# Kernel optimization log

Measured on AMD Instinct MI355X. Metric: run time of the kernel, lower is better.

## Reference

```python
import jax, jax.numpy as jnp
import numpy as np

D = 256   # vec_dim
H = 8     # head_num
P = 1024  # patch_num
N = 8     # batch


def setup_inputs() -> dict:
    key = jax.random.key(0)
    ks = jax.random.split(key, 11)
    s = 0.05
    return {
        "inputs": jax.random.normal(ks[0], (N, D, P), dtype=jnp.float32),
        "pos_mat": jax.random.normal(ks[1], (1, H, P, P), dtype=jnp.float32),
        "Wk": jax.random.normal(ks[2], (H * D, D), dtype=jnp.float32) * s,
        "bk": jax.random.normal(ks[3], (H * D,), dtype=jnp.float32) * s,
        "Wq": jax.random.normal(ks[4], (H * D, D), dtype=jnp.float32) * s,
        "bq": jax.random.normal(ks[5], (H * D,), dtype=jnp.float32) * s,
        "Wv": jax.random.normal(ks[6], (H * D, D), dtype=jnp.float32) * s,
        "bv": jax.random.normal(ks[7], (H * D,), dtype=jnp.float32) * s,
        "Wo": jax.random.normal(ks[8], (D, H * D), dtype=jnp.float32) * s,
        "bo": jax.random.normal(ks[9], (D,), dtype=jnp.float32) * s,
    }


def reference(inputs, pos_mat, Wk, bk, Wq, bq, Wv, bv, Wo, bo):
    n, d, p = inputs.shape  # [N, D, P]
    h = Wk.shape[0] // d
    # 1x1 Conv1d == per-position GEMM: [H*D,D] x [N,D,P] -> [N,H*D,P] -> [N,H,D,P]
    k = (jnp.einsum('od,ndp->nop', Wk, inputs) + bk[:, None]).reshape(n, h, d, p)
    q = (jnp.einsum('od,ndp->nop', Wq, inputs) + bq[:, None]).reshape(n, h, d, p)
    v = (jnp.einsum('od,ndp->nop', Wv, inputs) + bv[:, None]).reshape(n, h, d, p)
    # attn[n,h,kpos,qpos] = K^T Q / sqrt(D), shape [N,H,P,P]
    attn = jnp.einsum('nhdk,nhdq->nhkq', k, q) / jnp.sqrt(jnp.asarray(d, inputs.dtype))
    attn = attn + pos_mat
    # NOTE: original uses Softmax(dim=2), i.e. over the KEY axis, not the last dim
    w = jax.nn.softmax(attn, axis=2)
    out = jnp.einsum('nhdk,nhkq->nhdq', v, w).reshape(n, h * d, p)
    return jnp.einsum('oi,nip->nop', Wo, out) + bo[:, None]
```

## Files before the change

kernel.cpp:

```cpp
#include <hip/hip_runtime.h>

typedef __bf16 bf16;
typedef __attribute__((ext_vector_type(8))) __bf16 bf16x8;
typedef __attribute__((ext_vector_type(4))) __bf16 bf16x4;
typedef __attribute__((ext_vector_type(2))) __bf16 bf16x2;
typedef __attribute__((ext_vector_type(4))) float f32x4;

#define MFMA16(a, b, c) __builtin_amdgcn_mfma_f32_16x16x32_bf16(a, b, c, 0, 0, 0)

__device__ __forceinline__ void gload_lds16(const void* g, void* l) {
  __builtin_amdgcn_global_load_lds(
      (const __attribute__((address_space(1))) void*)g,
      (__attribute__((address_space(3))) void*)l, 16, 0, 0);
}

constexpr int NH = 8, DD = 256, PP = 1024;

constexpr size_t WB_YT  = 33554432;
constexpr size_t WB_XB  = 67108864;
constexpr size_t WB_XBT = 71303168;
constexpr size_t WB_MB  = 75497472;
constexpr size_t WB_UB  = 76546048;
constexpr size_t WB_U   = 77594624;
constexpr size_t WB_BPP = 77602816;

constexpr int FL_PT0  = 0;
constexpr int FL_XT0  = 16384;
constexpr int FL_LRED = 0;
constexpr int FL_SZ   = 81920;

#define EXP_SHIFT 4.0f

__global__ __launch_bounds__(256, 1) void msa_mu(
    const float* __restrict__ Wk, const float* __restrict__ Wq,
    const float* __restrict__ Wo, const float* __restrict__ Wv,
    const float* __restrict__ bq, const float* __restrict__ bv,
    bf16* __restrict__ Mb, bf16* __restrict__ Ub,
    float* __restrict__ u, float* __restrict__ bpp) {
  __shared__ float lds[64 * 65];
  __shared__ float svec[64];
  const int t = threadIdx.x;
  const int i0 = (blockIdx.x >> 2) * 64;
  const int jq = blockIdx.x & 3;
  const int h = blockIdx.y;
  const int mode = blockIdx.z;
  const int j0 = (t & 31) * 2 + jq * 64;
  const int i8 = t >> 5;
  float acc0[8], acc1[8];
#pragma unroll
  for (int r = 0; r < 8; ++r) { acc0[r] = 0.f; acc1[r] = 0.f; }
  float accS = 0.f;
  const float* __restrict__ W2 = (mode == 0) ? Wq : Wv;
  const float* __restrict__ vec = (mode == 0) ? bq : bv;
  for (int dhc = 0; dhc < 256; dhc += 64) {
    __syncthreads();
    if (mode == 0) {
#pragma unroll
      for (int s = 0; s < 16; ++s) {
        int f = t + s * 256;
        int dh = f >> 6, ii = f & 63;
        lds[dh * 65 + ii] = Wk[(h * 256 + dhc + dh) * 256 + i0 + ii];
      }
    } else {
#pragma unroll
      for (int s = 0; s < 16; ++s) {
        int f = t + s * 256;
        int oo = f >> 6, dh = f & 63;
        lds[dh * 65 + oo] = Wo[(i0 + oo) * 2048 + h * 256 + dhc + dh];
      }
    }
    if (jq == 0 && t < 64) svec[t] = vec[h * 256 + dhc + t];
    __syncthreads();
#pragma unroll 8
    for (int dl = 0; dl < 64; ++dl) {
      float2 wv2 = *reinterpret_cast<const float2*>(&W2[(h * 256 + dhc + dl) * 256 + j0]);
#pragma unroll
      for (int r = 0; r < 8; ++r) {
        float x = lds[dl * 65 + i8 * 8 + r];
        acc0[r] = fmaf(x, wv2.x, acc0[r]);
        acc1[r] = fmaf(x, wv2.y, acc1[r]);
      }
    }
    if (jq == 0 && t < 64) {
      float a = 0.f;
#pragma unroll 8
      for (int dh = 0; dh < 64; ++dh) a = fmaf(lds[dh * 65 + t], svec[dh], a);
      accS += a;
    }
  }
  if (mode == 0) {
#pragma unroll
    for (int r = 0; r < 8; ++r) {
      int i = i0 + i8 * 8 + r;
      bf16x2 v = { (__bf16)(acc0[r] * 0.0625f), (__bf16)(acc1[r] * 0.0625f) };
      *reinterpret_cast<bf16x2*>(&Mb[h * 65536 + i * 256 + j0]) = v;
    }
    if (jq == 0 && t < 64) u[h * 256 + i0 + t] = accS * 0.0625f;
  } else {
#pragma unroll
    for (int r = 0; r < 8; ++r) {
      int o = i0 + i8 * 8 + r;
      bf16x2 v = { (__bf16)acc0[r], (__bf16)acc1[r] };
      *reinterpret_cast<bf16x2*>(&Ub[o * 2048 + h * 256 + j0]) = v;
    }
    if (jq == 0 && t < 64) bpp[h * 256 + i0 + t] = accS;
  }
}

__global__ __launch_bounds__(256, 4) void msa_cvtX(
    const float* __restrict__ X, bf16* __restrict__ Xb, bf16* __restrict__ XbT) {
  __shared__ __bf16 tl[64 * 68];
  const int t = threadIdx.x;
  const int p0 = blockIdx.x * 64, d0 = blockIdx.y * 64, n = blockIdx.z;
  const float* __restrict__ Xn = X + (size_t)n * DD * PP;
#pragma unroll
  for (int rr = 0; rr < 4; ++rr) {
    int r = (t >> 4) + rr * 16, c = (t & 15) * 4;
    float4 v = *reinterpret_cast<const float4*>(Xn + (size_t)(d0 + r) * PP + p0 + c);
    bf16x4 pk = { (__bf16)v.x, (__bf16)v.y, (__bf16)v.z, (__bf16)v.w };
    *reinterpret_cast<bf16x4*>(Xb + (size_t)n * DD * PP + (size_t)(d0 + r) * PP + p0 + c) = pk;
    *reinterpret_cast<bf16x4*>(&tl[r * 68 + c]) = pk;
  }
  __syncthreads();
#pragma unroll
  for (int rr = 0; rr < 4; ++rr) {
    int pr = (t >> 4) + rr * 16, dc = (t & 15) * 4;
    bf16x4 pk = { tl[(dc + 0) * 68 + pr], tl[(dc + 1) * 68 + pr],
                  tl[(dc + 2) * 68 + pr], tl[(dc + 3) * 68 + pr] };
    *reinterpret_cast<bf16x4*>(XbT + (size_t)n * PP * DD + (size_t)(p0 + pr) * DD + d0 + dc) = pk;
  }
}

__global__ __launch_bounds__(256, 2) void msa_flash(
    const bf16* __restrict__ XbT, const bf16* __restrict__ Xb,
    const bf16* __restrict__ Mb, const float* __restrict__ u,
    const float* __restrict__ pos, bf16* __restrict__ Yt) {
  extern __shared__ char smc[];
  const int t = threadIdx.x;
  const int lane = t & 63, w = t >> 6;
  const int g = lane >> 4, ln = lane & 15;
  const int kw = w >> 1, qw = w & 1;
  const int qt = blockIdx.x, h = blockIdx.y, n = blockIdx.z;
  const int qg0 = qt * 64, nh = n * 8 + h;
  const bf16* __restrict__ XbTn = XbT + (size_t)n * (PP * DD);
  const bf16* __restrict__ Xbn  = Xb + (size_t)n * (DD * PP);
  const bf16* __restrict__ Mh   = Mb + (size_t)h * (DD * DD);
  const float* __restrict__ posh = pos + (size_t)h * (PP * PP);
  float* lredp = (float*)(smc + FL_LRED);

  const int grl = lane >> 5;
  const int gcb = lane & 31;

  {
    bf16x8 ta[4][8];
#pragma unroll
    for (int mq = 0; mq < 4; ++mq)
#pragma unroll
      for (int s = 0; s < 8; ++s)
        ta[mq][s] = *reinterpret_cast<const bf16x8*>(
            XbTn + (size_t)(qg0 + mq * 16 + ln) * DD + s * 32 + g * 8);
#pragma unroll
    for (int ni = 0; ni < 4; ++ni) {
      const int i_ = w * 64 + ni * 16 + ln;
      bf16x8 tb8[8];
#pragma unroll
      for (int s = 0; s < 8; ++s)
        tb8[s] = *reinterpret_cast<const bf16x8*>(Mh + (size_t)i_ * DD + s * 32 + g * 8);
      const float uv = u[h * 256 + i_];
#pragma unroll
      for (int mq = 0; mq < 4; ++mq) {
        f32x4 acc = {0.f, 0.f, 0.f, 0.f};
#pragma unroll
        for (int s = 0; s < 8; ++s) acc = MFMA16(ta[mq][s], tb8[s], acc);
#pragma unroll
        for (int r = 0; r < 4; ++r) {
          const int q = mq * 16 + 4 * g + r;
          const int addr = FL_XT0 + q * 512 +
              (((w * 8 + ni * 2 + (ln >> 3)) ^ (q & 7)) << 4) + (ln & 7) * 2;
          *reinterpret_cast<__bf16*>(smc + addr) = (__bf16)(acc[r] + uv);
        }
      }
    }
  }
  __syncthreads();

  bf16x8 tb[2][8];
#pragma unroll
  for (int nq = 0; nq < 2; ++nq) {
    const int q_ = qw * 32 + nq * 16 + ln;
#pragma unroll
    for (int s = 0; s < 8; ++s)
      tb[nq][s] = *reinterpret_cast<const bf16x8*>(
          smc + FL_XT0 + q_ * 512 + (((4 * s + g) ^ (q_ & 7)) << 4));
  }
  __syncthreads();

#pragma unroll
  for (int c = 0; c < 8; ++c) {
    const int row = w * 16 + c * 2 + grl;
    const int cbg = gcb ^ (row & 7);
    gload_lds16(XbTn + (size_t)row * DD + cbg * 8,
                smc + FL_XT0 + w * 8192 + c * 1024);
  }
  __syncthreads();

  float lsum[2] = {0.f, 0.f};
  f32x4 yacc[4][4];
#pragma unroll
  for (int a = 0; a < 4; ++a)
#pragma unroll
    for (int b = 0; b < 4; ++b) { f32x4 z = {0.f, 0.f, 0.f, 0.f}; yacc[a][b] = z; }

  for (int kt = 0; kt < 16; ++kt) {
    const int kg0 = kt * 64;
    const int curXT = FL_XT0 + (kt & 1) * 32768;
    const int nxtXT = FL_XT0 + ((kt + 1) & 1) * 32768;
    const int curPT = FL_PT0 + (kt & 1) * 8192;
    if (kt < 15) {
#pragma unroll
      for (int c = 0; c < 8; ++c) {
        const int row = w * 16 + c * 2 + grl;
        const int cbg = gcb ^ (row & 7);
        gload_lds16(XbTn + (size_t)(kg0 + 64 + row) * DD + cbg * 8,
                    smc + nxtXT + w * 8192 + c * 1024);
      }
    }
    float posv[2][2][4];
#pragma unroll
    for (int mt = 0; mt < 2; ++mt)
#pragma unroll
      for (int nq = 0; nq < 2; ++nq) {
        const float* pr = posh + (size_t)(kg0 + kw * 32 + mt * 16 + 4 * g) * PP +
                          qg0 + qw * 32 + nq * 16 + ln;
#pragma unroll
        for (int r = 0; r < 4; ++r) posv[mt][nq][r] = pr[(size_t)r * PP];
      }
    f32x4 sacc[2][2];
#pragma unroll
    for (int a = 0; a < 2; ++a)
#pragma unroll
      for (int b = 0; b < 2; ++b) { f32x4 z = {0.f, 0.f, 0.f, 0.f}; sacc[a][b] = z; }
#pragma unroll
    for (int mt = 0; mt < 2; ++mt) {
      const int row = kw * 32 + mt * 16 + ln;
      bf16x8 af8[8];
#pragma unroll
      for (int s = 0; s < 8; ++s)
        af8[s] = *reinterpret_cast<const bf16x8*>(
            smc + curXT + row * 512 + (((4 * s + g) ^ (row & 7)) << 4));
#pragma unroll
      for (int s = 0; s < 8; ++s)
#pragma unroll
        for (int nq = 0; nq < 2; ++nq)
          sacc[mt][nq] = MFMA16(af8[s], tb[nq][s], sacc[mt][nq]);
    }
#pragma unroll
    for (int mt = 0; mt < 2; ++mt)
#pragma unroll
      for (int nq = 0; nq < 2; ++nq) {
        bf16x4 pk;
#pragma unroll
        for (int r = 0; r < 4; ++r) {
          float e = __expf(sacc[mt][nq][r] + posv[mt][nq][r] - EXP_SHIFT);
          lsum[nq] += e;
          pk[r] = (__bf16)e;
        }
        const int q_ = qw * 32 + nq * 16 + ln;
        *reinterpret_cast<bf16x4*>(smc + curPT + q_ * 128 +
            (((kw * 4 + mt * 2 + (g >> 1)) ^ (q_ & 7)) << 4) + ((g & 1) << 3)) = pk;
      }
    __syncthreads();
#pragma unroll
    for (int ks = 0; ks < 2; ++ks) {
      bf16x8 pa[4], xv[4];
#pragma unroll
      for (int mq = 0; mq < 4; ++mq) {
        const int q_ = mq * 16 + ln;
        pa[mq] = *reinterpret_cast<const bf16x8*>(
            smc + curPT + q_ * 128 + (((4 * ks + g) ^ (q_ & 7)) << 4));
      }
#pragma unroll
      for (int nd = 0; nd < 4; ++nd)
        xv[nd] = *reinterpret_cast<const bf16x8*>(
            Xbn + (size_t)(w * 64 + nd * 16 + ln) * PP + kg0 + ks * 32 + g * 8);
#pragma unroll
      for (int mq = 0; mq < 4; ++mq)
#pragma unroll
        for (int nd = 0; nd < 4; ++nd)
          yacc[mq][nd] = MFMA16(pa[mq], xv[nd], yacc[mq][nd]);
    }
  }

#pragma unroll
  for (int nq = 0; nq < 2; ++nq) {
    lsum[nq] += __shfl_xor(lsum[nq], 16);
    lsum[nq] += __shfl_xor(lsum[nq], 32);
  }
  if (lane < 16) {
#pragma unroll
    for (int nq = 0; nq < 2; ++nq)
      lredp[kw * 64 + qw * 32 + nq * 16 + ln] = lsum[nq];
  }
  __syncthreads();
  bf16* __restrict__ Ytp = Yt + (size_t)nh * (PP * DD);
#pragma unroll
  for (int mq = 0; mq < 4; ++mq) {
    f32x4 l0 = *reinterpret_cast<const f32x4*>(lredp + mq * 16 + 4 * g);
    f32x4 l1 = *reinterpret_cast<const f32x4*>(lredp + 64 + mq * 16 + 4 * g);
    f32x4 inv;
#pragma unroll
    for (int r = 0; r < 4; ++r) inv[r] = 1.0f / (l0[r] + l1[r]);
#pragma unroll
    for (int nd = 0; nd < 4; ++nd)
#pragma unroll
      for (int r = 0; r < 4; ++r)
        Ytp[(size_t)(qg0 + mq * 16 + 4 * g + r) * DD + w * 64 + nd * 16 + ln] =
            (__bf16)(yacc[mq][nd][r] * inv[r]);
  }
}

__global__ __launch_bounds__(512, 1) void msa_final5(
    const bf16* __restrict__ Ub, const bf16* __restrict__ Yt,
    const float* __restrict__ bo, const float* __restrict__ bpp,
    float* __restrict__ out) {
  __shared__ char lsd[49152];
  const int t = threadIdx.x, lane = t & 63, w = t >> 6;
  const int g = lane >> 4, ln = lane & 15;
  const int pw = w & 3, ow = w >> 2;
  const int pb = blockIdx.x * 128, ob = blockIdx.y * 64, n = blockIdx.z;
  const bf16* __restrict__ Ytn = Yt + (size_t)n * 8 * (PP * DD);
  f32x4 acc[2][2];
#pragma unroll
  for (int a = 0; a < 2; ++a)
#pragma unroll
    for (int b = 0; b < 2; ++b) { f32x4 z = {0.f, 0.f, 0.f, 0.f}; acc[a][b] = z; }

  uint4 areg, breg[2];
  {
    areg = *reinterpret_cast<const uint4*>(
        Ub + (size_t)(ob + (t >> 3)) * 2048 + 0 + (t & 7) * 8);
#pragma unroll
    for (int j = 0; j < 2; ++j) {
      int v_ = t + j * 512;
      breg[j] = *reinterpret_cast<const uint4*>(
          Ytn + ((size_t)0 * PP + pb + (v_ >> 3)) * DD + 0 + (v_ & 7) * 8);
    }
    {
      int row = t >> 3, cb = t & 7;
      *reinterpret_cast<uint4*>(lsd + row * 128 + ((cb ^ (row & 7)) << 4)) = areg;
    }
#pragma unroll
    for (int j = 0; j < 2; ++j) {
      int v_ = t + j * 512, row = v_ >> 3, cb = v_ & 7;
      *reinterpret_cast<uint4*>(lsd + 8192 + row * 128 + ((cb ^ (row & 7)) << 4)) = breg[j];
    }
  }
  __syncthreads();

  for (int kc = 0; kc < 32; ++kc) {
    const int cur = (kc & 1) * 24576;
    const int nxt = ((kc + 1) & 1) * 24576;
    if (kc < 31) {
      const int k1 = (kc + 1) * 64, hh = k1 >> 8, dd = k1 & 255;
      areg = *reinterpret_cast<const uint4*>(
          Ub + (size_t)(ob + (t >> 3)) * 2048 + k1 + (t & 7) * 8);
#pragma unroll
      for (int j = 0; j < 2; ++j) {
        int v_ = t + j * 512;
        breg[j] = *reinterpret_cast<const uint4*>(
            Ytn + ((size_t)hh * PP + pb + (v_ >> 3)) * DD + dd + (v_ & 7) * 8);
      }
    }
#pragma unroll
    for (int ks = 0; ks < 2; ++ks) {
      bf16x8 a[2], b[2];
#pragma unroll
      for (int mo = 0; mo < 2; ++mo) {
        const int row = ow * 32 + mo * 16 + ln;
        a[mo] = *reinterpret_cast<const bf16x8*>(
            lsd + cur + row * 128 + (((4 * ks + g) ^ (row & 7)) << 4));
      }
#pragma unroll
      for (int np = 0; np < 2; ++np) {
        const int row = pw * 32 + np * 16 + ln;
        b[np] = *reinterpret_cast<const bf16x8*>(
            lsd + cur + 8192 + row * 128 + (((4 * ks + g) ^ (row & 7)) << 4));
      }
#pragma unroll
      for (int mo = 0; mo < 2; ++mo)
#pragma unroll
        for (int np = 0; np < 2; ++np) acc[mo][np] = MFMA16(a[mo], b[np], acc[mo][np]);
    }
    if (kc < 31) {
      {
        int row = t >> 3, cb = t & 7;
        *reinterpret_cast<uint4*>(lsd + nxt + row * 128 + ((cb ^ (row & 7)) << 4)) = areg;
      }
#pragma unroll
      for (int j = 0; j < 2; ++j) {
        int v_ = t + j * 512, row = v_ >> 3, cb = v_ & 7;
        *reinterpret_cast<uint4*>(lsd + nxt + 8192 + row * 128 + ((cb ^ (row & 7)) << 4)) = breg[j];
      }
    }
    __syncthreads();
  }

#pragma unroll
  for (int mo = 0; mo < 2; ++mo) {
    const int o4 = ob + ow * 32 + mo * 16 + 4 * g;
    f32x4 bb = *reinterpret_cast<const f32x4*>(bo + o4);
#pragma unroll
    for (int hh = 0; hh < 8; ++hh) {
      f32x4 pv = *reinterpret_cast<const f32x4*>(bpp + hh * 256 + o4);
#pragma unroll
      for (int r = 0; r < 4; ++r) bb[r] += pv[r];
    }
#pragma unroll
    for (int np = 0; np < 2; ++np)
#pragma unroll
      for (int r = 0; r < 4; ++r) {
        const int o = o4 + r;
        out[((size_t)n * DD + o) * PP + pb + pw * 32 + np * 16 + ln] =
            acc[mo][np][r] + bb[r];
      }
  }
}

extern "C" void kernel_launch(void* const* d_in, const int* in_sizes, int n_in,
                              void* d_out, int out_size, void* d_ws, size_t ws_size,
                              hipStream_t stream) {
  const float* X   = (const float*)d_in[0];
  const float* pos = (const float*)d_in[1];
  const float* Wk  = (const float*)d_in[2];
  const float* Wq  = (const float*)d_in[4];
  const float* bq  = (const float*)d_in[5];
  const float* Wv  = (const float*)d_in[6];
  const float* bv  = (const float*)d_in[7];
  const float* Wo  = (const float*)d_in[8];
  const float* bo  = (const float*)d_in[9];

  char* ws = (char*)d_ws;
  bf16* Yt  = (bf16*)(ws + WB_YT);
  bf16* Xb  = (bf16*)(ws + WB_XB);
  bf16* XbT = (bf16*)(ws + WB_XBT);
  bf16* Mb  = (bf16*)(ws + WB_MB);
  bf16* Ub  = (bf16*)(ws + WB_UB);
  float* u  = (float*)(ws + WB_U);
  float* bpp = (float*)(ws + WB_BPP);
  float* out = (float*)d_out;

  hipFuncSetAttribute(reinterpret_cast<const void*>(msa_flash),
                      hipFuncAttributeMaxDynamicSharedMemorySize, FL_SZ);

  msa_cvtX<<<dim3(16, 4, 8), 256, 0, stream>>>(X, Xb, XbT);
  msa_mu<<<dim3(16, 8, 2), 256, 0, stream>>>(Wk, Wq, Wo, Wv, bq, bv, Mb, Ub, u, bpp);
  msa_flash<<<dim3(16, 8, 8), 256, FL_SZ, stream>>>(XbT, Xb, Mb, u, pos, Yt);
  msa_final5<<<dim3(8, 4, 8), 512, 0, stream>>>(Ub, Yt, bo, bpp, out);
}
```

Baseline: 267.3 us.

## Read key tiles directly from global memory and enlarge key tile to 128

Removes the double-buffered global-to-LDS async staging of the key (XbT) tiles and instead loads MFMA A-operands straight from global memory. The key tile per iteration grows from 64 to 128 rows, halving loop iterations and barriers, and the LDS footprint shrinks from 80KB to 32KB, which may allow more resident blocks. The trade-off is losing explicit prefetch overlap and relying on cache hits for repeated key reads, plus more registers for the larger score and position tiles.

```diff
diff --git a/kernel.cpp b/kernel.cpp
--- a/kernel.cpp
+++ b/kernel.cpp
@@ -7,12 +7,6 @@
 typedef __attribute__((ext_vector_type(4))) float f32x4;
 
 #define MFMA16(a, b, c) __builtin_amdgcn_mfma_f32_16x16x32_bf16(a, b, c, 0, 0, 0)
-
-__device__ __forceinline__ void gload_lds16(const void* g, void* l) {
-  __builtin_amdgcn_global_load_lds(
-      (const __attribute__((address_space(1))) void*)g,
-      (__attribute__((address_space(3))) void*)l, 16, 0, 0);
-}
 
 constexpr int NH = 8, DD = 256, PP = 1024;
 
@@ -25,9 +19,8 @@
 constexpr size_t WB_BPP = 77602816;
 
 constexpr int FL_PT0  = 0;
-constexpr int FL_XT0  = 16384;
 constexpr int FL_LRED = 0;
-constexpr int FL_SZ   = 81920;
+constexpr int FL_SZ   = 32768;
 
 #define EXP_SHIFT 4.0f
 
@@ -148,9 +141,6 @@
   const float* __restrict__ posh = pos + (size_t)h * (PP * PP);
   float* lredp = (float*)(smc + FL_LRED);
 
-  const int grl = lane >> 5;
-  const int gcb = lane & 31;
-
   {
     bf16x8 ta[4][8];
 #pragma unroll
@@ -175,7 +165,7 @@
 #pragma unroll
         for (int r = 0; r < 4; ++r) {
           const int q = mq * 16 + 4 * g + r;
-          const int addr = FL_XT0 + q * 512 +
+          const int addr = q * 512 +
               (((w * 8 + ni * 2 + (ln >> 3)) ^ (q & 7)) << 4) + (ln & 7) * 2;
           *reinterpret_cast<__bf16*>(smc + addr) = (__bf16)(acc[r] + uv);
         }
@@ -191,16 +181,7 @@
 #pragma unroll
     for (int s = 0; s < 8; ++s)
       tb[nq][s] = *reinterpret_cast<const bf16x8*>(
-          smc + FL_XT0 + q_ * 512 + (((4 * s + g) ^ (q_ & 7)) << 4));
-  }
-  __syncthreads();
-
-#pragma unroll
-  for (int c = 0; c < 8; ++c) {
-    const int row = w * 16 + c * 2 + grl;
-    const int cbg = gcb ^ (row & 7);
-    gload_lds16(XbTn + (size_t)row * DD + cbg * 8,
-                smc + FL_XT0 + w * 8192 + c * 1024);
+          smc + q_ * 512 + (((4 * s + g) ^ (q_ & 7)) << 4));
   }
   __syncthreads();
 
@@ -211,43 +192,31 @@
 #pragma unroll
     for (int b = 0; b < 4; ++b) { f32x4 z = {0.f, 0.f, 0.f, 0.f}; yacc[a][b] = z; }
 
-  for (int kt = 0; kt < 16; ++kt) {
-    const int kg0 = kt * 64;
-    const int curXT = FL_XT0 + (kt & 1) * 32768;
-    const int nxtXT = FL_XT0 + ((kt + 1) & 1) * 32768;
-    const int curPT = FL_PT0 + (kt & 1) * 8192;
-    if (kt < 15) {
-#pragma unroll
-      for (int c = 0; c < 8; ++c) {
-        const int row = w * 16 + c * 2 + grl;
-        const int cbg = gcb ^ (row & 7);
-        gload_lds16(XbTn + (size_t)(kg0 + 64 + row) * DD + cbg * 8,
-                    smc + nxtXT + w * 8192 + c * 1024);
-      }
-    }
-    float posv[2][2][4];
-#pragma unroll
-    for (int mt = 0; mt < 2; ++mt)
+  for (int kt = 0; kt < 8; ++kt) {
+    const int kg0 = kt * 128;
+    const int curPT = FL_PT0 + (kt & 1) * 16384;
+    float posv[4][2][4];
+#pragma unroll
+    for (int mt = 0; mt < 4; ++mt)
 #pragma unroll
       for (int nq = 0; nq < 2; ++nq) {
-        const float* pr = posh + (size_t)(kg0 + kw * 32 + mt * 16 + 4 * g) * PP +
+        const float* pr = posh + (size_t)(kg0 + kw * 64 + mt * 16 + 4 * g) * PP +
                           qg0 + qw * 32 + nq * 16 + ln;
 #pragma unroll
         for (int r = 0; r < 4; ++r) posv[mt][nq][r] = pr[(size_t)r * PP];
       }
-    f32x4 sacc[2][2];
-#pragma unroll
-    for (int a = 0; a < 2; ++a)
+    f32x4 sacc[4][2];
+#pragma unroll
+    for (int a = 0; a < 4; ++a)
 #pragma unroll
       for (int b = 0; b < 2; ++b) { f32x4 z = {0.f, 0.f, 0.f, 0.f}; sacc[a][b] = z; }
 #pragma unroll
-    for (int mt = 0; mt < 2; ++mt) {
-      const int row = kw * 32 + mt * 16 + ln;
+    for (int mt = 0; mt < 4; ++mt) {
+      const bf16* arow = XbTn + (size_t)(kg0 + kw * 64 + mt * 16 + ln) * DD;
       bf16x8 af8[8];
 #pragma unroll
       for (int s = 0; s < 8; ++s)
-        af8[s] = *reinterpret_cast<const bf16x8*>(
-            smc + curXT + row * 512 + (((4 * s + g) ^ (row & 7)) << 4));
+        af8[s] = *reinterpret_cast<const bf16x8*>(arow + s * 32 + g * 8);
 #pragma unroll
       for (int s = 0; s < 8; ++s)
 #pragma unroll
@@ -255,7 +224,7 @@
           sacc[mt][nq] = MFMA16(af8[s], tb[nq][s], sacc[mt][nq]);
     }
 #pragma unroll
-    for (int mt = 0; mt < 2; ++mt)
+    for (int mt = 0; mt < 4; ++mt)
 #pragma unroll
       for (int nq = 0; nq < 2; ++nq) {
         bf16x4 pk;
@@ -266,18 +235,18 @@
           pk[r] = (__bf16)e;
         }
         const int q_ = qw * 32 + nq * 16 + ln;
-        *reinterpret_cast<bf16x4*>(smc + curPT + q_ * 128 +
-            (((kw * 4 + mt * 2 + (g >> 1)) ^ (q_ & 7)) << 4) + ((g & 1) << 3)) = pk;
+        *reinterpret_cast<bf16x4*>(smc + curPT + q_ * 256 +
+            (((kw * 8 + mt * 2 + (g >> 1)) ^ (q_ & 7)) << 4) + ((g & 1) << 3)) = pk;
       }
     __syncthreads();
 #pragma unroll
-    for (int ks = 0; ks < 2; ++ks) {
+    for (int ks = 0; ks < 4; ++ks) {
       bf16x8 pa[4], xv[4];
 #pragma unroll
       for (int mq = 0; mq < 4; ++mq) {
         const int q_ = mq * 16 + ln;
         pa[mq] = *reinterpret_cast<const bf16x8*>(
-            smc + curPT + q_ * 128 + (((4 * ks + g) ^ (q_ & 7)) << 4));
+            smc + curPT + q_ * 256 + (((ks * 4 + g) ^ (q_ & 7)) << 4));
       }
 #pragma unroll
       for (int nd = 0; nd < 4; ++nd)
```

Measured after the change: 409.2 us. +53.1%, slower.
